# Performance work log

Hardware: AMD Instinct MI355X
Metric: run time of the kernel (lower is better)

## Reference

```python
import jax, jax.numpy as jnp
import numpy as np

N, D, H = 8192, 256, 64  # n_nodes, feature dim, MLP hidden
DENSITY = 0.01


def setup_inputs() -> dict:
    key = jax.random.key(0)
    k1, k2, k3, k4, k5 = jax.random.split(key, 5)
    vals = jax.random.uniform(k1, (N, N), dtype=jnp.float32)
    mask = jax.random.uniform(k2, (N, N)) < DENSITY
    graph_info = jnp.where(mask, vals, 0.0)
    h = jax.random.normal(k3, (N, D), dtype=jnp.float32)
    W1 = jax.random.normal(k4, (D, H), dtype=jnp.float32) * (1.0 / np.sqrt(D))
    b1 = jnp.zeros((H,), dtype=jnp.float32)
    W2 = jax.random.normal(k5, (H, 1), dtype=jnp.float32) * (1.0 / np.sqrt(H))
    b2 = jnp.zeros((1,), dtype=jnp.float32)
    return {"graph_info": graph_info, "h": h, "W1": W1, "b1": b1, "W2": W2, "b2": b2}


def reference(graph_info, h, W1, b1, W2, b2):
    # weight_forwaed: inter==0 so no P interaction; MLP(dims->64->1) + sigmoid
    e = jax.nn.sigmoid(jax.nn.relu(h @ W1 + b1) @ W2 + b2)  # [N, 1], per-node gate
    # torch: graph_info_1 = spmm(A^T, I)^T == dense(A); e^T repeated over rows ->
    # att[i, j] = e[j] if A[i, j] > 0 else 0
    att = jnp.where(graph_info > 0, e[:, 0][None, :], jnp.float32(0.0))  # [N, N]
    h_out = att @ h  # [N, D] aggregation (second spmm)
    return (h_out, e)
```

## Files before the change

### kernel.cpp

```cpp
#include <hip/hip_runtime.h>
#include <math.h>


__global__ __launch_bounds__(256) void gate_kernel(const float* __restrict__ h,
                                                   const float* __restrict__ W1,
                                                   const float* __restrict__ b1,
                                                   const float* __restrict__ W2,
                                                   const float* __restrict__ b2,
                                                   float* __restrict__ e_out,
                                                   int N) {
    __shared__ float W1s[256 * 64];
    const int tid = threadIdx.x;

    const float4* W1v = reinterpret_cast<const float4*>(W1);
    float4* W1sv = reinterpret_cast<float4*>(W1s);
    #pragma unroll
    for (int t = 0; t < 16; ++t) W1sv[tid + 256 * t] = W1v[tid + 256 * t];
    __syncthreads();

    const int wave = tid >> 6;
    const int k    = tid & 63;
    const float b1k = b1[k];
    const float w2k = W2[k];
    const float b2v = b2[0];

    const int base = blockIdx.x * 16;
    for (int r = wave; r < 16; r += 4) {
        const int i = base + r;
        if (i >= N) break;
        const float4* hv = reinterpret_cast<const float4*>(h + (size_t)i * 256);
        float acc = 0.f;
        #pragma unroll 4
        for (int d4 = 0; d4 < 64; ++d4) {
            float4 a = hv[d4];
            const int d = d4 * 4;
            acc = fmaf(a.x, W1s[(d + 0) * 64 + k], acc);
            acc = fmaf(a.y, W1s[(d + 1) * 64 + k], acc);
            acc = fmaf(a.z, W1s[(d + 2) * 64 + k], acc);
            acc = fmaf(a.w, W1s[(d + 3) * 64 + k], acc);
        }
        float v = fmaxf(acc + b1k, 0.f) * w2k;
        #pragma unroll
        for (int off = 32; off > 0; off >>= 1) v += __shfl_down(v, off);
        if (k == 0) e_out[i] = 1.f / (1.f + expf(-(v + b2v)));
    }
}

__global__ __launch_bounds__(256) void agg_kernel(const float* __restrict__ A,
                                                  const float* __restrict__ h,
                                                  const float* __restrict__ e,
                                                  float* __restrict__ h_out,
                                                  int N) {
    const int tid  = threadIdx.x;
    const int lane = tid & 63;
    const int i    = blockIdx.x * 4 + (tid >> 6);
    if (i >= N) return;

    const float4* Arow = reinterpret_cast<const float4*>(A + (size_t)i * N);
    const float4* hv   = reinterpret_cast<const float4*>(h);

    float4 acc = {0.f, 0.f, 0.f, 0.f};
    const int groups = N / 256;
    for (int g = 0; g < groups; ++g) {
        float4 a4 = Arow[g * 64 + lane];
        unsigned long long mx = __ballot(a4.x > 0.f);
        unsigned long long my = __ballot(a4.y > 0.f);
        unsigned long long mz = __ballot(a4.z > 0.f);
        unsigned long long mw = __ballot(a4.w > 0.f);
        const int jb = g * 256;

        while (mx) { int b = __builtin_ctzll(mx); mx &= mx - 1;
            int j = jb + 4 * b + 0; float ej = e[j]; float4 hj = hv[(size_t)j * 64 + lane];
            acc.x = fmaf(ej, hj.x, acc.x); acc.y = fmaf(ej, hj.y, acc.y);
            acc.z = fmaf(ej, hj.z, acc.z); acc.w = fmaf(ej, hj.w, acc.w); }
        while (my) { int b = __builtin_ctzll(my); my &= my - 1;
            int j = jb + 4 * b + 1; float ej = e[j]; float4 hj = hv[(size_t)j * 64 + lane];
            acc.x = fmaf(ej, hj.x, acc.x); acc.y = fmaf(ej, hj.y, acc.y);
            acc.z = fmaf(ej, hj.z, acc.z); acc.w = fmaf(ej, hj.w, acc.w); }
        while (mz) { int b = __builtin_ctzll(mz); mz &= mz - 1;
            int j = jb + 4 * b + 2; float ej = e[j]; float4 hj = hv[(size_t)j * 64 + lane];
            acc.x = fmaf(ej, hj.x, acc.x); acc.y = fmaf(ej, hj.y, acc.y);
            acc.z = fmaf(ej, hj.z, acc.z); acc.w = fmaf(ej, hj.w, acc.w); }
        while (mw) { int b = __builtin_ctzll(mw); mw &= mw - 1;
            int j = jb + 4 * b + 3; float ej = e[j]; float4 hj = hv[(size_t)j * 64 + lane];
            acc.x = fmaf(ej, hj.x, acc.x); acc.y = fmaf(ej, hj.y, acc.y);
            acc.z = fmaf(ej, hj.z, acc.z); acc.w = fmaf(ej, hj.w, acc.w); }
    }

    float4* outv = reinterpret_cast<float4*>(h_out + (size_t)i * 256);
    outv[lane] = acc;
}

extern "C" void kernel_launch(void* const* d_in, const int* in_sizes, int n_in,
                              void* d_out, int out_size, void* d_ws, size_t ws_size,
                              hipStream_t stream) {
    const float* A  = (const float*)d_in[0];
    const float* h  = (const float*)d_in[1];
    const float* W1 = (const float*)d_in[2];
    const float* b1 = (const float*)d_in[3];
    const float* W2 = (const float*)d_in[4];
    const float* b2 = (const float*)d_in[5];

    const int H = in_sizes[3];
    const int D = in_sizes[2] / H;
    const int N = in_sizes[1] / D;

    float* out   = (float*)d_out;
    float* h_out = out;
    float* e_out = out + (size_t)N * D;

    gate_kernel<<<(N + 15) / 16, 256, 0, stream>>>(h, W1, b1, W2, b2, e_out, N);
    agg_kernel<<<(N + 3) / 4, 256, 0, stream>>>(A, h, e_out, h_out, N);
}
```

Measured before the change: 420.0 us.

## Prescale h by gate, prefetch adjacency nontemporally, interleave gathers across columns

The gate kernel now writes a prescaled copy g = e*h into the workspace, so the aggregation no longer needs a per-edge load of e or a multiply. The aggregation kernel software-prefetches the next adjacency chunk with nontemporal loads and processes the four ballot masks together, issuing up to four independent row gathers per iteration to raise memory-level parallelism. The output is written with nontemporal stores. This adds an extra N×D write and read through the workspace and more register pressure in exchange for fewer dependent loads.

```diff
diff --git a/kernel.cpp b/kernel.cpp
--- a/kernel.cpp
+++ b/kernel.cpp
@@ -1,6 +1,8 @@
 #include <hip/hip_runtime.h>
 #include <math.h>
 
+
+typedef float nfloat4 __attribute__((ext_vector_type(4)));
 
 __global__ __launch_bounds__(256) void gate_kernel(const float* __restrict__ h,
                                                    const float* __restrict__ W1,
@@ -8,6 +10,7 @@
                                                    const float* __restrict__ W2,
                                                    const float* __restrict__ b2,
                                                    float* __restrict__ e_out,
+                                                   float* __restrict__ g_out,
                                                    int N) {
     __shared__ float W1s[256 * 64];
     const int tid = threadIdx.x;
@@ -42,13 +45,17 @@
         float v = fmaxf(acc + b1k, 0.f) * w2k;
         #pragma unroll
         for (int off = 32; off > 0; off >>= 1) v += __shfl_down(v, off);
-        if (k == 0) e_out[i] = 1.f / (1.f + expf(-(v + b2v)));
+        float vs = __shfl(v, 0);
+        float ev = 1.f / (1.f + expf(-(vs + b2v)));
+        if (k == 0) e_out[i] = ev;
+        float4 hr = hv[k];
+        float4* gv = reinterpret_cast<float4*>(g_out + (size_t)i * 256);
+        gv[k] = make_float4(ev * hr.x, ev * hr.y, ev * hr.z, ev * hr.w);
     }
 }
 
 __global__ __launch_bounds__(256) void agg_kernel(const float* __restrict__ A,
-                                                  const float* __restrict__ h,
-                                                  const float* __restrict__ e,
+                                                  const float* __restrict__ g,
                                                   float* __restrict__ h_out,
                                                   int N) {
     const int tid  = threadIdx.x;
@@ -56,39 +63,46 @@
     const int i    = blockIdx.x * 4 + (tid >> 6);
     if (i >= N) return;
 
-    const float4* Arow = reinterpret_cast<const float4*>(A + (size_t)i * N);
-    const float4* hv   = reinterpret_cast<const float4*>(h);
+    const nfloat4* Arow = reinterpret_cast<const nfloat4*>(A + (size_t)i * N);
+    const float4*  gv   = reinterpret_cast<const float4*>(g);
 
     float4 acc = {0.f, 0.f, 0.f, 0.f};
     const int groups = N / 256;
-    for (int g = 0; g < groups; ++g) {
-        float4 a4 = Arow[g * 64 + lane];
+
+    nfloat4 a4 = __builtin_nontemporal_load(&Arow[lane]);
+    for (int gi = 0; gi < groups; ++gi) {
+        nfloat4 a_next;
+        if (gi + 1 < groups)
+            a_next = __builtin_nontemporal_load(&Arow[(gi + 1) * 64 + lane]);
+
         unsigned long long mx = __ballot(a4.x > 0.f);
         unsigned long long my = __ballot(a4.y > 0.f);
         unsigned long long mz = __ballot(a4.z > 0.f);
         unsigned long long mw = __ballot(a4.w > 0.f);
-        const int jb = g * 256;
+        const int jb = gi * 256;
 
-        while (mx) { int b = __builtin_ctzll(mx); mx &= mx - 1;
-            int j = jb + 4 * b + 0; float ej = e[j]; float4 hj = hv[(size_t)j * 64 + lane];
-            acc.x = fmaf(ej, hj.x, acc.x); acc.y = fmaf(ej, hj.y, acc.y);
-            acc.z = fmaf(ej, hj.z, acc.z); acc.w = fmaf(ej, hj.w, acc.w); }
-        while (my) { int b = __builtin_ctzll(my); my &= my - 1;
-            int j = jb + 4 * b + 1; float ej = e[j]; float4 hj = hv[(size_t)j * 64 + lane];
-            acc.x = fmaf(ej, hj.x, acc.x); acc.y = fmaf(ej, hj.y, acc.y);
-            acc.z = fmaf(ej, hj.z, acc.z); acc.w = fmaf(ej, hj.w, acc.w); }
-        while (mz) { int b = __builtin_ctzll(mz); mz &= mz - 1;
-            int j = jb + 4 * b + 2; float ej = e[j]; float4 hj = hv[(size_t)j * 64 + lane];
-            acc.x = fmaf(ej, hj.x, acc.x); acc.y = fmaf(ej, hj.y, acc.y);
-            acc.z = fmaf(ej, hj.z, acc.z); acc.w = fmaf(ej, hj.w, acc.w); }
-        while (mw) { int b = __builtin_ctzll(mw); mw &= mw - 1;
-            int j = jb + 4 * b + 3; float ej = e[j]; float4 hj = hv[(size_t)j * 64 + lane];
-            acc.x = fmaf(ej, hj.x, acc.x); acc.y = fmaf(ej, hj.y, acc.y);
-            acc.z = fmaf(ej, hj.z, acc.z); acc.w = fmaf(ej, hj.w, acc.w); }
+        while (mx | my | mz | mw) {
+            float4 hx, hy, hz, hw;
+            bool px = mx != 0, py = my != 0, pz = mz != 0, pw = mw != 0;
+            if (px) { int b = __builtin_ctzll(mx); mx &= mx - 1;
+                      hx = gv[(size_t)(jb + 4 * b + 0) * 64 + lane]; }
+            if (py) { int b = __builtin_ctzll(my); my &= my - 1;
+                      hy = gv[(size_t)(jb + 4 * b + 1) * 64 + lane]; }
+            if (pz) { int b = __builtin_ctzll(mz); mz &= mz - 1;
+                      hz = gv[(size_t)(jb + 4 * b + 2) * 64 + lane]; }
+            if (pw) { int b = __builtin_ctzll(mw); mw &= mw - 1;
+                      hw = gv[(size_t)(jb + 4 * b + 3) * 64 + lane]; }
+            if (px) { acc.x += hx.x; acc.y += hx.y; acc.z += hx.z; acc.w += hx.w; }
+            if (py) { acc.x += hy.x; acc.y += hy.y; acc.z += hy.z; acc.w += hy.w; }
+            if (pz) { acc.x += hz.x; acc.y += hz.y; acc.z += hz.z; acc.w += hz.w; }
+            if (pw) { acc.x += hw.x; acc.y += hw.y; acc.z += hw.z; acc.w += hw.w; }
+        }
+        a4 = a_next;
     }
 
-    float4* outv = reinterpret_cast<float4*>(h_out + (size_t)i * 256);
-    outv[lane] = acc;
+    nfloat4 r; r.x = acc.x; r.y = acc.y; r.z = acc.z; r.w = acc.w;
+    nfloat4* outv = reinterpret_cast<nfloat4*>(h_out + (size_t)i * 256);
+    __builtin_nontemporal_store(r, &outv[lane]);
 }
 
 extern "C" void kernel_launch(void* const* d_in, const int* in_sizes, int n_in,
@@ -108,7 +122,8 @@
     float* out   = (float*)d_out;
     float* h_out = out;
     float* e_out = out + (size_t)N * D;
+    float* g_buf = (float*)d_ws;
 
-    gate_kernel<<<(N + 15) / 16, 256, 0, stream>>>(h, W1, b1, W2, b2, e_out, N);
-    agg_kernel<<<(N + 3) / 4, 256, 0, stream>>>(A, h, e_out, h_out, N);
+    gate_kernel<<<(N + 15) / 16, 256, 0, stream>>>(h, W1, b1, W2, b2, e_out, g_buf, N);
+    agg_kernel<<<(N + 3) / 4, 256, 0, stream>>>(A, g_buf, h_out, N);
 }
```

Measured after the change: 410.3 us. 1.02x faster.
